# Kernel optimization log

Measured on AMD Instinct MI355X. Metric: run time of the kernel, lower is better.

Reference implementation:

```python
import jax, jax.numpy as jnp
import numpy as np

UNITS = 512
INPUT_DIM = 64
BATCH = 131072


def setup_inputs() -> dict:
    key = jax.random.key(0)
    kx, kw = jax.random.split(key)
    x = jax.random.normal(kx, (BATCH, INPUT_DIM), dtype=jnp.float32)
    w = jax.random.normal(kw, (UNITS, INPUT_DIM), dtype=jnp.float32) * 0.05
    return {"x": x, "w": w}


def reference(x, w):
    # Pairwise squared L2 distance: dist[b, u] = sum_d (w[u,d] - x[b,d])^2
    # avoids the O(B*U*D) broadcast intermediate).
    x_sq = jnp.sum(x * x, axis=-1, keepdims=True)        # [B, 1]
    w_sq = jnp.sum(w * w, axis=-1)[None, :]              # [1, U]
    cross = jnp.einsum("bd,ud->bu", x, w)                # [B, U]
    return x_sq + w_sq - 2.0 * cross
```

## Files before the change

kernel.cpp:

```cpp
#include <hip/hip_runtime.h>

#define BATCH 131072
#define UNITS 512
#define DIM   64
#define BM    128
#define TILES 2
#define NFRAG 4096

typedef __attribute__((ext_vector_type(8))) short  short8;
typedef __attribute__((ext_vector_type(4))) float  floatx4;

static __device__ __forceinline__ unsigned short f32_to_bf16(float f) {
    union { float f; unsigned int u; } c; c.f = f;
    unsigned int u = c.u;
    unsigned int r = u + 0x7fffu + ((u >> 16) & 1u);
    return (unsigned short)(r >> 16);
}

__global__ __launch_bounds__(256) void prep_wsq_kernel(
    const float* __restrict__ w, float* __restrict__ wsq)
{
    const int u = blockIdx.x * 4 + (threadIdx.x >> 6);
    const int d = threadIdx.x & 63;
    float v = w[u * DIM + d];
    float s = v * v;
    #pragma unroll
    for (int o = 32; o > 0; o >>= 1) s += __shfl_xor(s, o);
    if (d == 0) wsq[u] = s;
}

__global__ __launch_bounds__(256) void prep_wfrag_kernel(
    const float* __restrict__ w, uint4* __restrict__ wbf)
{
    const int tid  = blockIdx.x * 256 + threadIdx.x;
    const int lane = tid & 63;
    const int fi   = tid >> 6;
    const int h    = fi & 1;
    const int tt   = fi >> 1;
    const int u    = (tt >> 2) * 64 + (tt & 3) * 16 + (lane & 15);
    const int k0   = h * 32 + (lane >> 4) * 8;
    const float* src = w + u * DIM + k0;
    float v[8];
    *(float4*)&v[0] = *(const float4*)src;
    *(float4*)&v[4] = *(const float4*)(src + 4);
    unsigned short p[8];
    #pragma unroll
    for (int i = 0; i < 8; ++i) p[i] = f32_to_bf16(v[i]);
    wbf[tid] = *(uint4*)p;
}

__global__ __launch_bounds__(256, 2) void dist_kernel(
    const float* __restrict__ x,
    const uint4* __restrict__ wbf,
    const float* __restrict__ wsq,
    float* __restrict__ out)
{
    __shared__ __align__(16) uint4 wbs[NFRAG];
    __shared__ __align__(16) float wsq_s[UNITS];

    const int tid  = threadIdx.x;
    const int wave = tid >> 6;
    const int lane = tid & 63;
    const int l15  = lane & 15;
    const int quad = lane >> 4;
    const int mrow = wave * 32;
    const int row0 = blockIdx.x * (BM * TILES);

    #pragma unroll 4
    for (int i = 0; i < 16; ++i)
        wbs[i * 256 + tid] = wbf[i * 256 + tid];
    wsq_s[tid]       = wsq[tid];
    wsq_s[tid + 256] = wsq[tid + 256];

    short8 a[TILES][2][2];
    float  xs2[TILES][2];
    #pragma unroll
    for (int tl = 0; tl < TILES; ++tl) {
        #pragma unroll
        for (int mf = 0; mf < 2; ++mf) {
            const float* xr = x + (size_t)(row0 + tl * BM + mrow + mf * 16 + l15) * DIM;
            float v[16];
            *(float4*)&v[0]  = *(const float4*)(xr + quad * 8);
            *(float4*)&v[4]  = *(const float4*)(xr + quad * 8 + 4);
            *(float4*)&v[8]  = *(const float4*)(xr + 32 + quad * 8);
            *(float4*)&v[12] = *(const float4*)(xr + 32 + quad * 8 + 4);
            float s = 0.f;
            unsigned short p[16];
            #pragma unroll
            for (int i = 0; i < 16; ++i) { s += v[i] * v[i]; p[i] = f32_to_bf16(v[i]); }
            a[tl][mf][0] = *(short8*)&p[0];
            a[tl][mf][1] = *(short8*)&p[8];
            s += __shfl_xor(s, 16);
            s += __shfl_xor(s, 32);
            xs2[tl][mf] = s;
        }
    }
    __syncthreads();

    #pragma unroll
    for (int tl = 0; tl < TILES; ++tl) {
        for (int gu = 0; gu < 8; ++gu) {
            const int colb = gu * 64;

            short8  b[4][2];
            floatx4 wq[4];
            #pragma unroll
            for (int t = 0; t < 4; ++t) {
                const int fb = ((gu * 4 + t) * 2) * 64 + lane;
                uint4 r0 = wbs[fb];
                uint4 r1 = wbs[fb + 64];
                b[t][0] = *(short8*)&r0;
                b[t][1] = *(short8*)&r1;
                wq[t]   = *(const floatx4*)&wsq_s[colb + t * 16 + quad * 4];
            }

            #pragma unroll
            for (int mf = 0; mf < 2; ++mf) {
                #pragma unroll
                for (int t = 0; t < 4; ++t) {
                    floatx4 acc = floatx4{0.f, 0.f, 0.f, 0.f};
                    acc = __builtin_amdgcn_mfma_f32_16x16x32_bf16(b[t][0], a[tl][mf][0], acc, 0, 0, 0);
                    acc = __builtin_amdgcn_mfma_f32_16x16x32_bf16(b[t][1], a[tl][mf][1], acc, 0, 0, 0);

                    floatx4 vo;
                    #pragma unroll
                    for (int i = 0; i < 4; ++i)
                        vo[i] = xs2[tl][mf] + wq[t][i] - 2.0f * acc[i];

                    float* dst = out + (size_t)(row0 + tl * BM + mrow + mf * 16 + l15) * UNITS
                                     + colb + t * 16 + quad * 4;
                    *(floatx4*)dst = vo;
                }
            }
        }
    }
}

extern "C" void kernel_launch(void* const* d_in, const int* in_sizes, int n_in,
                              void* d_out, int out_size, void* d_ws, size_t ws_size,
                              hipStream_t stream) {
    const float* x = (const float*)d_in[0];
    const float* w = (const float*)d_in[1];
    float* out = (float*)d_out;

    uint4* wbf = (uint4*)d_ws;
    float* wsq = (float*)((char*)d_ws + NFRAG * sizeof(uint4));

    prep_wsq_kernel<<<UNITS / 4, 256, 0, stream>>>(w, wsq);
    prep_wfrag_kernel<<<NFRAG / 256, 256, 0, stream>>>(w, wbf);
    dist_kernel<<<BATCH / (BM * TILES), 256, 0, stream>>>(x, wbf, wsq, out);
}
```

Baseline: 313.0 us.

## Stage output tiles through LDS for row-contiguous stores and use 512-thread blocks

```diff
diff --git a/kernel.cpp b/kernel.cpp
--- a/kernel.cpp
+++ b/kernel.cpp
@@ -3,9 +3,9 @@
 #define BATCH 131072
 #define UNITS 512
 #define DIM   64
-#define BM    128
-#define TILES 2
+#define BROWS 256
 #define NFRAG 4096
+#define STRIDE 68
 
 typedef __attribute__((ext_vector_type(8))) short  short8;
 typedef __attribute__((ext_vector_type(4))) float  floatx4;
@@ -49,7 +49,7 @@
     wbf[tid] = *(uint4*)p;
 }
 
-__global__ __launch_bounds__(256, 2) void dist_kernel(
+__global__ __launch_bounds__(512, 2) void dist_kernel(
     const float* __restrict__ x,
     const uint4* __restrict__ wbf,
     const float* __restrict__ wsq,
@@ -57,6 +57,7 @@
 {
     __shared__ __align__(16) uint4 wbs[NFRAG];
     __shared__ __align__(16) float wsq_s[UNITS];
+    __shared__ __align__(16) float st[8][16][STRIDE];
 
     const int tid  = threadIdx.x;
     const int wave = tid >> 6;
@@ -64,73 +65,78 @@
     const int l15  = lane & 15;
     const int quad = lane >> 4;
     const int mrow = wave * 32;
-    const int row0 = blockIdx.x * (BM * TILES);
+    const int row0 = blockIdx.x * BROWS;
 
-    #pragma unroll 4
-    for (int i = 0; i < 16; ++i)
-        wbs[i * 256 + tid] = wbf[i * 256 + tid];
-    wsq_s[tid]       = wsq[tid];
-    wsq_s[tid + 256] = wsq[tid + 256];
+    #pragma unroll
+    for (int i = 0; i < 8; ++i)
+        wbs[i * 512 + tid] = wbf[i * 512 + tid];
+    wsq_s[tid] = wsq[tid];
 
-    short8 a[TILES][2][2];
-    float  xs2[TILES][2];
+    short8 a[2][2];
+    float  xs[2][4];
     #pragma unroll
-    for (int tl = 0; tl < TILES; ++tl) {
+    for (int mf = 0; mf < 2; ++mf) {
+        const float* xr = x + (size_t)(row0 + mrow + mf * 16 + l15) * DIM;
+        float v[16];
+        *(float4*)&v[0]  = *(const float4*)(xr + quad * 8);
+        *(float4*)&v[4]  = *(const float4*)(xr + quad * 8 + 4);
+        *(float4*)&v[8]  = *(const float4*)(xr + 32 + quad * 8);
+        *(float4*)&v[12] = *(const float4*)(xr + 32 + quad * 8 + 4);
+        float s = 0.f;
+        unsigned short p[16];
         #pragma unroll
-        for (int mf = 0; mf < 2; ++mf) {
-            const float* xr = x + (size_t)(row0 + tl * BM + mrow + mf * 16 + l15) * DIM;
-            float v[16];
-            *(float4*)&v[0]  = *(const float4*)(xr + quad * 8);
-            *(float4*)&v[4]  = *(const float4*)(xr + quad * 8 + 4);
-            *(float4*)&v[8]  = *(const float4*)(xr + 32 + quad * 8);
-            *(float4*)&v[12] = *(const float4*)(xr + 32 + quad * 8 + 4);
-            float s = 0.f;
-            unsigned short p[16];
-            #pragma unroll
-            for (int i = 0; i < 16; ++i) { s += v[i] * v[i]; p[i] = f32_to_bf16(v[i]); }
-            a[tl][mf][0] = *(short8*)&p[0];
-            a[tl][mf][1] = *(short8*)&p[8];
-            s += __shfl_xor(s, 16);
-            s += __shfl_xor(s, 32);
-            xs2[tl][mf] = s;
-        }
+        for (int i = 0; i < 16; ++i) { s += v[i] * v[i]; p[i] = f32_to_bf16(v[i]); }
+        a[mf][0] = *(short8*)&p[0];
+        a[mf][1] = *(short8*)&p[8];
+        s += __shfl_xor(s, 16);
+        s += __shfl_xor(s, 32);
+        #pragma unroll
+        for (int i = 0; i < 4; ++i)
+            xs[mf][i] = __shfl(s, quad * 4 + i);
     }
     __syncthreads();
 
-    #pragma unroll
-    for (int tl = 0; tl < TILES; ++tl) {
-        for (int gu = 0; gu < 8; ++gu) {
-            const int colb = gu * 64;
+    float* stw = &st[wave][0][0];
 
-            short8  b[4][2];
-            floatx4 wq[4];
+    for (int gu = 0; gu < 8; ++gu) {
+        const int colb = gu * 64;
+
+        short8 b[4][2];
+        float  wq[4];
+        #pragma unroll
+        for (int t = 0; t < 4; ++t) {
+            const int fb = ((gu * 4 + t) * 2) * 64 + lane;
+            uint4 r0 = wbs[fb];
+            uint4 r1 = wbs[fb + 64];
+            b[t][0] = *(short8*)&r0;
+            b[t][1] = *(short8*)&r1;
+            wq[t]   = wsq_s[colb + t * 16 + l15];
+        }
+
+        #pragma unroll
+        for (int mf = 0; mf < 2; ++mf) {
+            floatx4 acc[4];
             #pragma unroll
             for (int t = 0; t < 4; ++t) {
-                const int fb = ((gu * 4 + t) * 2) * 64 + lane;
-                uint4 r0 = wbs[fb];
-                uint4 r1 = wbs[fb + 64];
-                b[t][0] = *(short8*)&r0;
-                b[t][1] = *(short8*)&r1;
-                wq[t]   = *(const floatx4*)&wsq_s[colb + t * 16 + quad * 4];
+                acc[t] = floatx4{0.f, 0.f, 0.f, 0.f};
+                acc[t] = __builtin_amdgcn_mfma_f32_16x16x32_bf16(a[mf][0], b[t][0], acc[t], 0, 0, 0);
+                acc[t] = __builtin_amdgcn_mfma_f32_16x16x32_bf16(a[mf][1], b[t][1], acc[t], 0, 0, 0);
             }
 
             #pragma unroll
-            for (int mf = 0; mf < 2; ++mf) {
+            for (int t = 0; t < 4; ++t)
                 #pragma unroll
-                for (int t = 0; t < 4; ++t) {
-                    floatx4 acc = floatx4{0.f, 0.f, 0.f, 0.f};
-                    acc = __builtin_amdgcn_mfma_f32_16x16x32_bf16(b[t][0], a[tl][mf][0], acc, 0, 0, 0);
-                    acc = __builtin_amdgcn_mfma_f32_16x16x32_bf16(b[t][1], a[tl][mf][1], acc, 0, 0, 0);
+                for (int i = 0; i < 4; ++i)
+                    stw[(quad * 4 + i) * STRIDE + t * 16 + l15] =
+                        xs[mf][i] + wq[t] - 2.0f * acc[t][i];
 
-                    floatx4 vo;
-                    #pragma unroll
-                    for (int i = 0; i < 4; ++i)
-                        vo[i] = xs2[tl][mf] + wq[t][i] - 2.0f * acc[i];
-
-                    float* dst = out + (size_t)(row0 + tl * BM + mrow + mf * 16 + l15) * UNITS
-                                     + colb + t * 16 + quad * 4;
-                    *(floatx4*)dst = vo;
-                }
+            #pragma unroll
+            for (int j = 0; j < 4; ++j) {
+                const int r = quad + 4 * j;
+                const floatx4 v = *(const floatx4*)&stw[r * STRIDE + l15 * 4];
+                float* dst = out + (size_t)(row0 + mrow + mf * 16 + r) * UNITS
+                                 + colb + l15 * 4;
+                *(floatx4*)dst = v;
             }
         }
     }
@@ -148,5 +154,5 @@
 
     prep_wsq_kernel<<<UNITS / 4, 256, 0, stream>>>(w, wsq);
     prep_wfrag_kernel<<<NFRAG / 256, 256, 0, stream>>>(w, wbf);
-    dist_kernel<<<BATCH / (BM * TILES), 256, 0, stream>>>(x, wbf, wsq, out);
+    dist_kernel<<<BATCH / BROWS, 512, 0, stream>>>(x, wbf, wsq, out);
 }
```

New measurement: 298.1 us. -4.8%, faster.

## Split units across blocks to halve LDS per block and raise occupancy

Applied to the files above, without the earlier changes.

```diff
diff --git a/kernel.cpp b/kernel.cpp
--- a/kernel.cpp
+++ b/kernel.cpp
@@ -4,7 +4,6 @@
 #define UNITS 512
 #define DIM   64
 #define BM    128
-#define TILES 2
 #define NFRAG 4096
 
 typedef __attribute__((ext_vector_type(8))) short  short8;
@@ -49,88 +48,80 @@
     wbf[tid] = *(uint4*)p;
 }
 
-__global__ __launch_bounds__(256, 2) void dist_kernel(
+__global__ __launch_bounds__(256, 4) void dist_kernel(
     const float* __restrict__ x,
     const uint4* __restrict__ wbf,
     const float* __restrict__ wsq,
     float* __restrict__ out)
 {
-    __shared__ __align__(16) uint4 wbs[NFRAG];
-    __shared__ __align__(16) float wsq_s[UNITS];
+    __shared__ __align__(16) uint4 wbs[2048];
+    __shared__ __align__(16) float wsq_s[256];
 
     const int tid  = threadIdx.x;
     const int wave = tid >> 6;
     const int lane = tid & 63;
     const int l15  = lane & 15;
     const int quad = lane >> 4;
-    const int mrow = wave * 32;
-    const int row0 = blockIdx.x * (BM * TILES);
 
-    #pragma unroll 4
-    for (int i = 0; i < 16; ++i)
-        wbs[i * 256 + tid] = wbf[i * 256 + tid];
-    wsq_s[tid]       = wsq[tid];
-    wsq_s[tid + 256] = wsq[tid + 256];
+    const int bid  = blockIdx.x;
+    const int ch   = bid >> 10;
+    const int rb   = bid & 1023;
+    const int row0 = rb * BM;
 
-    short8 a[TILES][2][2];
-    float  xs2[TILES][2];
     #pragma unroll
-    for (int tl = 0; tl < TILES; ++tl) {
+    for (int i = 0; i < 8; ++i)
+        wbs[i * 256 + tid] = wbf[ch * 2048 + i * 256 + tid];
+    wsq_s[tid] = wsq[ch * 256 + tid];
+
+    short8 a[2][2];
+    float  xs2[2];
+    #pragma unroll
+    for (int mf = 0; mf < 2; ++mf) {
+        const float* xr = x + (size_t)(row0 + wave * 32 + mf * 16 + l15) * DIM;
+        float v[16];
+        *(float4*)&v[0]  = *(const float4*)(xr + quad * 8);
+        *(float4*)&v[4]  = *(const float4*)(xr + quad * 8 + 4);
+        *(float4*)&v[8]  = *(const float4*)(xr + 32 + quad * 8);
+        *(float4*)&v[12] = *(const float4*)(xr + 32 + quad * 8 + 4);
+        float s = 0.f;
+        unsigned short p[16];
         #pragma unroll
-        for (int mf = 0; mf < 2; ++mf) {
-            const float* xr = x + (size_t)(row0 + tl * BM + mrow + mf * 16 + l15) * DIM;
-            float v[16];
-            *(float4*)&v[0]  = *(const float4*)(xr + quad * 8);
-            *(float4*)&v[4]  = *(const float4*)(xr + quad * 8 + 4);
-            *(float4*)&v[8]  = *(const float4*)(xr + 32 + quad * 8);
-            *(float4*)&v[12] = *(const float4*)(xr + 32 + quad * 8 + 4);
-            float s = 0.f;
-            unsigned short p[16];
-            #pragma unroll
-            for (int i = 0; i < 16; ++i) { s += v[i] * v[i]; p[i] = f32_to_bf16(v[i]); }
-            a[tl][mf][0] = *(short8*)&p[0];
-            a[tl][mf][1] = *(short8*)&p[8];
-            s += __shfl_xor(s, 16);
-            s += __shfl_xor(s, 32);
-            xs2[tl][mf] = s;
-        }
+        for (int i = 0; i < 16; ++i) { s += v[i] * v[i]; p[i] = f32_to_bf16(v[i]); }
+        a[mf][0] = *(short8*)&p[0];
+        a[mf][1] = *(short8*)&p[8];
+        s += __shfl_xor(s, 16);
+        s += __shfl_xor(s, 32);
+        xs2[mf] = s;
     }
     __syncthreads();
 
-    #pragma unroll
-    for (int tl = 0; tl < TILES; ++tl) {
-        for (int gu = 0; gu < 8; ++gu) {
-            const int colb = gu * 64;
+    const int   rowb = row0 + wave * 32;
+    float*      outb = out + (size_t)ch * 256;
 
-            short8  b[4][2];
-            floatx4 wq[4];
-            #pragma unroll
-            for (int t = 0; t < 4; ++t) {
-                const int fb = ((gu * 4 + t) * 2) * 64 + lane;
-                uint4 r0 = wbs[fb];
-                uint4 r1 = wbs[fb + 64];
-                b[t][0] = *(short8*)&r0;
-                b[t][1] = *(short8*)&r1;
-                wq[t]   = *(const floatx4*)&wsq_s[colb + t * 16 + quad * 4];
-            }
+    for (int g = 0; g < 4; ++g) {
+        #pragma unroll
+        for (int t = 0; t < 4; ++t) {
+            const int fb = ((g * 4 + t) * 2) * 64 + lane;
+            uint4 r0 = wbs[fb];
+            uint4 r1 = wbs[fb + 64];
+            const short8 b0 = *(short8*)&r0;
+            const short8 b1 = *(short8*)&r1;
+            const floatx4 wq = *(const floatx4*)&wsq_s[g * 64 + t * 16 + quad * 4];
 
             #pragma unroll
             for (int mf = 0; mf < 2; ++mf) {
+                floatx4 acc = floatx4{0.f, 0.f, 0.f, 0.f};
+                acc = __builtin_amdgcn_mfma_f32_16x16x32_bf16(b0, a[mf][0], acc, 0, 0, 0);
+                acc = __builtin_amdgcn_mfma_f32_16x16x32_bf16(b1, a[mf][1], acc, 0, 0, 0);
+
+                floatx4 vo;
                 #pragma unroll
-                for (int t = 0; t < 4; ++t) {
-                    floatx4 acc = floatx4{0.f, 0.f, 0.f, 0.f};
-                    acc = __builtin_amdgcn_mfma_f32_16x16x32_bf16(b[t][0], a[tl][mf][0], acc, 0, 0, 0);
-                    acc = __builtin_amdgcn_mfma_f32_16x16x32_bf16(b[t][1], a[tl][mf][1], acc, 0, 0, 0);
+                for (int i = 0; i < 4; ++i)
+                    vo[i] = xs2[mf] + wq[i] - 2.0f * acc[i];
 
-                    floatx4 vo;
-                    #pragma unroll
-                    for (int i = 0; i < 4; ++i)
-                        vo[i] = xs2[tl][mf] + wq[t][i] - 2.0f * acc[i];
-
-                    float* dst = out + (size_t)(row0 + tl * BM + mrow + mf * 16 + l15) * UNITS
-                                     + colb + t * 16 + quad * 4;
-                    *(floatx4*)dst = vo;
-                }
+                float* dst = outb + (size_t)(rowb + mf * 16 + l15) * UNITS
+                                  + g * 64 + t * 16 + quad * 4;
+                *(floatx4*)dst = vo;
             }
         }
     }
@@ -148,5 +139,5 @@
 
     prep_wsq_kernel<<<UNITS / 4, 256, 0, stream>>>(w, wsq);
     prep_wfrag_kernel<<<NFRAG / 256, 256, 0, stream>>>(w, wbf);
-    dist_kernel<<<BATCH / (BM * TILES), 256, 0, stream>>>(x, wbf, wsq, out);
+    dist_kernel<<<2 * (BATCH / BM), 256, 0, stream>>>(x, wbf, wsq, out);
 }
```

After: 301.8 us. -3.6%, faster.
